# Performance work log

Measured on AMD Instinct MI355X. Metric: run time of the kernel, lower is better.

## Reference

```python
import jax, jax.numpy as jnp
import numpy as np

N = 100000
E = 640000
D = 128      # node_dim == edge_dim
H = 256      # conv MLP hidden dim
EPS = 1e-5


def _ln(x, g, b):
    mu = jnp.mean(x, axis=-1, keepdims=True)
    var = jnp.var(x, axis=-1, keepdims=True)
    return (x - mu) * jax.lax.rsqrt(var + EPS) * g + b


def _conv_mlp(x, W1, b1, g1, be1, W2, b2, g2, be2):
    h = _ln(x @ W1 + b1, g1, be1)          # (N, H)
    h = jax.nn.relu(h)
    return _ln(h @ W2 + b2, g2, be2)        # (N, D)


def setup_inputs() -> dict:
    key = jax.random.key(0)
    ks = jax.random.split(key, 6)
    s1 = 1.0 / np.sqrt(D)
    s2 = 1.0 / np.sqrt(H)
    return {
        "x": jax.random.normal(ks[0], (N, D), dtype=jnp.float32),
        "edge_index": jax.random.randint(ks[1], (2, E), 0, N, dtype=jnp.int32),
        "edge_attr": jax.random.normal(ks[2], (E, D), dtype=jnp.float32),
        "W1": jax.random.uniform(ks[3], (D, H), jnp.float32, -s1, s1),
        "b1": jnp.zeros((H,), jnp.float32),
        "g1": jnp.ones((H,), jnp.float32),
        "be1": jnp.zeros((H,), jnp.float32),
        "W2": jax.random.uniform(ks[4], (H, D), jnp.float32, -s2, s2),
        "b2": jnp.zeros((D,), jnp.float32),
        "g2": jnp.ones((D,), jnp.float32),
        "be2": jnp.zeros((D,), jnp.float32),
        "g_out": jnp.ones((D,), jnp.float32),
        "b_out": jnp.zeros((D,), jnp.float32),
    }


def reference(x, edge_index, edge_attr, W1, b1, g1, be1, W2, b2, g2, be2, g_out, b_out):
    # Conv(h[w]) for all nodes once, then gather per edge (vectorized form of
    # the per-node/per-neighbor loops in the torch module).
    conv = _conv_mlp(x, W1, b1, g1, be1, W2, b2, g2, be2)   # (N, D)
    src, dst = edge_index[0], edge_index[1]
    msgs = conv[dst] * edge_attr                            # (E, D): Conv(h[w]) * e[v,w]
    agg = jax.ops.segment_sum(msgs, src, num_segments=N)    # scatter-add into v
    return _ln(agg + x, g_out, b_out)
```

## Files before the change

kernel.cpp:

```cpp
#include <hip/hip_runtime.h>

constexpr int D = 128;
constexpr int H = 256;
constexpr float EPS = 1e-5f;

typedef __attribute__((ext_vector_type(8))) __bf16  bf16x8;
typedef __attribute__((ext_vector_type(4))) float   f32x4;

static __device__ __forceinline__ unsigned short f2bfu(float f) {
    unsigned u = __float_as_uint(f);
    return (unsigned short)((u + 0x7FFFu + ((u >> 16) & 1u)) >> 16);
}
static __device__ __forceinline__ float bf2f(unsigned short u) {
    return __uint_as_float((unsigned)u << 16);
}

static __device__ __forceinline__ f32x4 mfma16x16x32(bf16x8 a, bf16x8 b, f32x4 c) {
    return __builtin_amdgcn_mfma_f32_16x16x32_bf16(a, b, c, 0, 0, 0);
}

__global__ __launch_bounds__(256) void pack_w_kernel(
    const float* __restrict__ W, unsigned short* __restrict__ Wp, int K, int Ncols)
{
    int e = blockIdx.x * 256 + threadIdx.x;
    if (e >= K * Ncols) return;
    int i  = e & 7;
    int l  = (e >> 3) & 63;
    int jt = e >> 9;
    int nt = K >> 5;
    int j  = jt / nt;
    int t  = jt - j * nt;
    int k  = 32 * t + ((l >> 4) << 3) + i;
    int c  = 16 * j + (l & 15);
    Wp[e] = f2bfu(W[(size_t)k * Ncols + c]);
}

__global__ __launch_bounds__(256) void conv_mlp_mfma(
    const float* __restrict__ x,
    const unsigned short* __restrict__ W1p, const float* __restrict__ b1,
    const float* __restrict__ g1, const float* __restrict__ be1,
    const unsigned short* __restrict__ W2p, const float* __restrict__ b2,
    const float* __restrict__ g2, const float* __restrict__ be2,
    unsigned short* __restrict__ convb, int N)
{
    __shared__ unsigned short Hs[64 * 256];
    const int wv   = threadIdx.x >> 6;
    const int lane = threadIdx.x & 63;
    const int rrow = lane & 15;
    const int kgrp = lane >> 4;
    const int r0   = blockIdx.x * 64 + wv * 16;

    int arow = r0 + rrow; if (arow >= N) arow = N - 1;
    const float* xr = x + (size_t)arow * D + kgrp * 8;
    bf16x8 A1[4];
    #pragma unroll
    for (int t = 0; t < 4; ++t) {
        float4 fa = *(const float4*)(xr + t * 32);
        float4 fb = *(const float4*)(xr + t * 32 + 4);
        bf16x8 a;
        a[0] = (__bf16)fa.x; a[1] = (__bf16)fa.y; a[2] = (__bf16)fa.z; a[3] = (__bf16)fa.w;
        a[4] = (__bf16)fb.x; a[5] = (__bf16)fb.y; a[6] = (__bf16)fb.z; a[7] = (__bf16)fb.w;
        A1[t] = a;
    }

    f32x4 acc[16];
    #pragma unroll
    for (int j = 0; j < 16; ++j) acc[j] = (f32x4){0.f, 0.f, 0.f, 0.f};
    const bf16x8* w1f = (const bf16x8*)W1p;
    #pragma unroll
    for (int j = 0; j < 16; ++j) {
        #pragma unroll
        for (int t = 0; t < 4; ++t) {
            bf16x8 B = w1f[(j * 4 + t) * 64 + lane];
            acc[j] = mfma16x16x32(A1[t], B, acc[j]);
        }
    }

    float b1r[16], g1r[16], be1r[16];
    #pragma unroll
    for (int j = 0; j < 16; ++j) {
        int c = 16 * j + rrow;
        b1r[j] = b1[c]; g1r[j] = g1[c]; be1r[j] = be1[c];
    }

    float s1[4] = {0,0,0,0}, s2[4] = {0,0,0,0};
    #pragma unroll
    for (int j = 0; j < 16; ++j) {
        #pragma unroll
        for (int r = 0; r < 4; ++r) {
            float v = acc[j][r] + b1r[j];
            acc[j][r] = v;
            s1[r] += v; s2[r] += v * v;
        }
    }
    #pragma unroll
    for (int m = 1; m < 16; m <<= 1) {
        #pragma unroll
        for (int r = 0; r < 4; ++r) {
            s1[r] += __shfl_xor(s1[r], m);
            s2[r] += __shfl_xor(s2[r], m);
        }
    }

    #pragma unroll
    for (int r = 0; r < 4; ++r) {
        float mu  = s1[r] * (1.f / H);
        float var = s2[r] * (1.f / H) - mu * mu;
        float rs  = rsqrtf(var + EPS);
        int row = wv * 16 + kgrp * 4 + r;
        #pragma unroll
        for (int j = 0; j < 16; ++j) {
            float h = fmaxf((acc[j][r] - mu) * rs * g1r[j] + be1r[j], 0.f);
            int byte = (row << 9) + ((16 * j + rrow) << 1);
            byte ^= (row & 15) << 4;
            *(unsigned short*)((char*)Hs + byte) = f2bfu(h);
        }
    }

    bf16x8 A2[8];
    #pragma unroll
    for (int t = 0; t < 8; ++t) {
        int row  = wv * 16 + rrow;
        int byte = (row << 9) + ((t * 32 + kgrp * 8) << 1);
        byte ^= (row & 15) << 4;
        A2[t] = *(const bf16x8*)((const char*)Hs + byte);
    }

    f32x4 acc2[8];
    #pragma unroll
    for (int j = 0; j < 8; ++j) acc2[j] = (f32x4){0.f, 0.f, 0.f, 0.f};
    const bf16x8* w2f = (const bf16x8*)W2p;
    #pragma unroll
    for (int j = 0; j < 8; ++j) {
        #pragma unroll
        for (int t = 0; t < 8; ++t) {
            bf16x8 B = w2f[(j * 8 + t) * 64 + lane];
            acc2[j] = mfma16x16x32(A2[t], B, acc2[j]);
        }
    }

    float b2r[8], g2r[8], be2r[8];
    #pragma unroll
    for (int j = 0; j < 8; ++j) {
        int c = 16 * j + rrow;
        b2r[j] = b2[c]; g2r[j] = g2[c]; be2r[j] = be2[c];
    }

    float u1[4] = {0,0,0,0}, u2[4] = {0,0,0,0};
    #pragma unroll
    for (int j = 0; j < 8; ++j) {
        #pragma unroll
        for (int r = 0; r < 4; ++r) {
            float v = acc2[j][r] + b2r[j];
            acc2[j][r] = v;
            u1[r] += v; u2[r] += v * v;
        }
    }
    #pragma unroll
    for (int m = 1; m < 16; m <<= 1) {
        #pragma unroll
        for (int r = 0; r < 4; ++r) {
            u1[r] += __shfl_xor(u1[r], m);
            u2[r] += __shfl_xor(u2[r], m);
        }
    }
    #pragma unroll
    for (int r = 0; r < 4; ++r) {
        float mu  = u1[r] * (1.f / D);
        float var = u2[r] * (1.f / D) - mu * mu;
        float rs  = rsqrtf(var + EPS);
        int grow = r0 + kgrp * 4 + r;
        if (grow < N) {
            #pragma unroll
            for (int j = 0; j < 8; ++j) {
                float o = (acc2[j][r] - mu) * rs * g2r[j] + be2r[j];
                convb[(size_t)grow * D + 16 * j + rrow] = f2bfu(o);
            }
        }
    }
}

__global__ __launch_bounds__(256) void zero_int_kernel(int* __restrict__ p, int n) {
    int i = blockIdx.x * blockDim.x + threadIdx.x;
    if (i < n) p[i] = 0;
}

__global__ __launch_bounds__(256) void hist_kernel(
    const int* __restrict__ eidx, int* __restrict__ counts, int E)
{
    int e = blockIdx.x * blockDim.x + threadIdx.x;
    if (e < E) atomicAdd(&counts[eidx[e]], 1);
}

__global__ __launch_bounds__(256) void scan1_kernel(
    const int* __restrict__ counts, int* __restrict__ row_start,
    int* __restrict__ bsums, int N)
{
    __shared__ int sd[256];
    int t  = threadIdx.x;
    int i0 = blockIdx.x * 1024 + t * 4;
    int c0 = (i0+0 < N) ? counts[i0+0] : 0;
    int c1 = (i0+1 < N) ? counts[i0+1] : 0;
    int c2 = (i0+2 < N) ? counts[i0+2] : 0;
    int c3 = (i0+3 < N) ? counts[i0+3] : 0;
    int s  = c0 + c1 + c2 + c3;
    sd[t] = s;
    __syncthreads();
    #pragma unroll
    for (int off = 1; off < 256; off <<= 1) {
        int v = (t >= off) ? sd[t - off] : 0;
        __syncthreads();
        sd[t] += v;
        __syncthreads();
    }
    int ex = sd[t] - s;
    if (i0+0 < N) row_start[i0+0] = ex;
    if (i0+1 < N) row_start[i0+1] = ex + c0;
    if (i0+2 < N) row_start[i0+2] = ex + c0 + c1;
    if (i0+3 < N) row_start[i0+3] = ex + c0 + c1 + c2;
    if (t == 255) bsums[blockIdx.x] = sd[255];
}

__global__ __launch_bounds__(128) void scan2_kernel(int* __restrict__ bsums, int NB)
{
    __shared__ int sd[128];
    int t = threadIdx.x;
    int v = (t < NB) ? bsums[t] : 0;
    sd[t] = v;
    __syncthreads();
    #pragma unroll
    for (int off = 1; off < 128; off <<= 1) {
        int u = (t >= off) ? sd[t - off] : 0;
        __syncthreads();
        sd[t] += u;
        __syncthreads();
    }
    if (t < NB) bsums[t] = sd[t] - v;
}

__global__ __launch_bounds__(256) void scan3_kernel(
    int* __restrict__ row_start, const int* __restrict__ bsums,
    int* __restrict__ cursor, int N)
{
    int i = blockIdx.x * blockDim.x + threadIdx.x;
    if (i < N) {
        int r = row_start[i] + bsums[i >> 10];
        row_start[i] = r;
        cursor[i]    = r;
    }
}

__global__ __launch_bounds__(256) void fill_kernel(
    const int* __restrict__ eidx, int* __restrict__ cursor,
    int2* __restrict__ edat, int E)
{
    int e = blockIdx.x * blockDim.x + threadIdx.x;
    if (e < E) {
        int s = eidx[e];
        int p = atomicAdd(&cursor[s], 1);
        edat[p] = make_int2(e, eidx[E + e]);
    }
}

__global__ __launch_bounds__(256) void gather_ln_kernel(
    const float* __restrict__ x, const unsigned short* __restrict__ convb,
    const float* __restrict__ eattr,
    const int* __restrict__ row_start, const int2* __restrict__ edat,
    const float* __restrict__ g, const float* __restrict__ b,
    float* __restrict__ out, int N, int E)
{
    int node = blockIdx.x * 4 + (threadIdx.x >> 6);
    if (node >= N) return;
    int lane = threadIdx.x & 63;
    int half = lane >> 5;
    int c4   = (lane & 31) * 4;

    float4 acc = make_float4(0.f, 0.f, 0.f, 0.f);
    int je = (node + 1 < N) ? row_start[node + 1] : E;
    int j  = row_start[node] + half;

    for (; j + 2 < je; j += 4) {
        int2 ea = edat[j];
        int2 eb = edat[j + 2];
        ushort4 ca = *(const ushort4*)(convb + (size_t)ea.y * D + c4);
        float4  aa = *(const float4*) (eattr + (size_t)ea.x * D + c4);
        ushort4 cb = *(const ushort4*)(convb + (size_t)eb.y * D + c4);
        float4  ab = *(const float4*) (eattr + (size_t)eb.x * D + c4);
        acc.x += bf2f(ca.x) * aa.x; acc.y += bf2f(ca.y) * aa.y;
        acc.z += bf2f(ca.z) * aa.z; acc.w += bf2f(ca.w) * aa.w;
        acc.x += bf2f(cb.x) * ab.x; acc.y += bf2f(cb.y) * ab.y;
        acc.z += bf2f(cb.z) * ab.z; acc.w += bf2f(cb.w) * ab.w;
    }
    if (j < je) {
        int2 ea = edat[j];
        ushort4 ca = *(const ushort4*)(convb + (size_t)ea.y * D + c4);
        float4  aa = *(const float4*) (eattr + (size_t)ea.x * D + c4);
        acc.x += bf2f(ca.x) * aa.x; acc.y += bf2f(ca.y) * aa.y;
        acc.z += bf2f(ca.z) * aa.z; acc.w += bf2f(ca.w) * aa.w;
    }

    if (half == 0) {
        float4 xv = *(const float4*)(x + (size_t)node * D + c4);
        acc.x += xv.x; acc.y += xv.y; acc.z += xv.z; acc.w += xv.w;
    }
    acc.x += __shfl_xor(acc.x, 32);
    acc.y += __shfl_xor(acc.y, 32);
    acc.z += __shfl_xor(acc.z, 32);
    acc.w += __shfl_xor(acc.w, 32);

    float s1 = acc.x + acc.y + acc.z + acc.w;
    float s2 = acc.x*acc.x + acc.y*acc.y + acc.z*acc.z + acc.w*acc.w;
    #pragma unroll
    for (int o = 1; o < 32; o <<= 1) {
        s1 += __shfl_xor(s1, o);
        s2 += __shfl_xor(s2, o);
    }
    float mu  = s1 * (1.f / D);
    float var = s2 * (1.f / D) - mu * mu;
    float rs  = rsqrtf(var + EPS);
    if (half == 0) {
        float4 gv = *(const float4*)(g + c4);
        float4 bv = *(const float4*)(b + c4);
        float4 o4;
        o4.x = (acc.x - mu) * rs * gv.x + bv.x;
        o4.y = (acc.y - mu) * rs * gv.y + bv.y;
        o4.z = (acc.z - mu) * rs * gv.z + bv.z;
        o4.w = (acc.w - mu) * rs * gv.w + bv.w;
        *(float4*)(out + (size_t)node * D + c4) = o4;
    }
}

extern "C" void kernel_launch(void* const* d_in, const int* in_sizes, int n_in,
                              void* d_out, int out_size, void* d_ws, size_t ws_size,
                              hipStream_t stream) {
    const float* x     = (const float*)d_in[0];
    const int*   eidx  = (const int*)  d_in[1];
    const float* eattr = (const float*)d_in[2];
    const float* W1    = (const float*)d_in[3];
    const float* b1    = (const float*)d_in[4];
    const float* g1    = (const float*)d_in[5];
    const float* be1   = (const float*)d_in[6];
    const float* W2    = (const float*)d_in[7];
    const float* b2    = (const float*)d_in[8];
    const float* g2    = (const float*)d_in[9];
    const float* be2   = (const float*)d_in[10];
    const float* g_out = (const float*)d_in[11];
    const float* b_out = (const float*)d_in[12];

    const int N = in_sizes[0] / D;
    const int E = in_sizes[1] / 2;

    float* out = (float*)d_out;

    auto align_up = [](size_t v) { return (v + 255) & ~(size_t)255; };
    size_t convB = align_up((size_t)N * D * sizeof(unsigned short));
    size_t cntB  = align_up((size_t)N * sizeof(int));
    size_t rsB   = align_up((size_t)N * sizeof(int));
    size_t bsB   = align_up(128 * sizeof(int));
    size_t edB   = align_up((size_t)E * sizeof(int2));
    size_t w1B   = align_up((size_t)D * H * sizeof(unsigned short));

    char* w = (char*)d_ws;
    unsigned short* convb     = (unsigned short*)(w);
    int*            counts    = (int*)(w + convB);
    int*            row_start = (int*)(w + convB + cntB);
    int*            bsums     = (int*)(w + convB + cntB + rsB);
    int2*           edat      = (int2*)(w + convB + cntB + rsB + bsB);
    unsigned short* W1p       = (unsigned short*)(w + convB + cntB + rsB + bsB + edB);
    unsigned short* W2p       = (unsigned short*)(w + convB + cntB + rsB + bsB + edB + w1B);

    pack_w_kernel<<<(D * H + 255) / 256, 256, 0, stream>>>(W1, W1p, D, H);
    pack_w_kernel<<<(H * D + 255) / 256, 256, 0, stream>>>(W2, W2p, H, D);

    conv_mlp_mfma<<<(N + 63) / 64, 256, 0, stream>>>(
        x, W1p, b1, g1, be1, W2p, b2, g2, be2, convb, N);

    zero_int_kernel<<<(N + 255) / 256, 256, 0, stream>>>(counts, N);
    hist_kernel<<<(E + 255) / 256, 256, 0, stream>>>(eidx, counts, E);
    int NB = (N + 1023) / 1024;
    scan1_kernel<<<NB, 256, 0, stream>>>(counts, row_start, bsums, N);
    scan2_kernel<<<1, 128, 0, stream>>>(bsums, NB);
    scan3_kernel<<<(N + 255) / 256, 256, 0, stream>>>(row_start, bsums, counts, N);
    fill_kernel<<<(E + 255) / 256, 256, 0, stream>>>(eidx, counts, edat, E);

    gather_ln_kernel<<<(N + 3) / 4, 256, 0, stream>>>(
        x, convb, eattr, row_start, edat, g_out, b_out, out, N, E);
}
```

Before: 230.2 us.

## Fuse weight packing, zeroing, conv+histogram and scan into fewer launches

Weight packing and zeroing of the count buffer are merged into one prep kernel. The conv MLP and the edge-degree histogram now run as one horizontally fused kernel, with blocks dispatched by block index, so the histogram overlaps the MLP. The three-pass prefix scan is replaced by a single 1024-thread block in which each thread serially scans a contiguous chunk, and the cursor now aliases the counts buffer. This cuts the number of launches, but the single-block scan serializes about 100 strided loads per thread, and the histogram blocks now carry the conv kernel's LDS allocation.

New measurement: 432.2 us. 87.8% more time.

```diff
diff --git a/kernel.cpp b/kernel.cpp
--- a/kernel.cpp
+++ b/kernel.cpp
@@ -19,11 +19,9 @@
     return __builtin_amdgcn_mfma_f32_16x16x32_bf16(a, b, c, 0, 0, 0);
 }
 
-__global__ __launch_bounds__(256) void pack_w_kernel(
-    const float* __restrict__ W, unsigned short* __restrict__ Wp, int K, int Ncols)
-{
-    int e = blockIdx.x * 256 + threadIdx.x;
-    if (e >= K * Ncols) return;
+static __device__ __forceinline__ void pack_w_elem(
+    const float* __restrict__ W, unsigned short* __restrict__ Wp, int K, int Ncols, int e)
+{
     int i  = e & 7;
     int l  = (e >> 3) & 63;
     int jt = e >> 9;
@@ -35,20 +33,36 @@
     Wp[e] = f2bfu(W[(size_t)k * Ncols + c]);
 }
 
-__global__ __launch_bounds__(256) void conv_mlp_mfma(
+__global__ __launch_bounds__(256) void prep_kernel(
+    const float* __restrict__ W1, unsigned short* __restrict__ W1p,
+    const float* __restrict__ W2, unsigned short* __restrict__ W2p,
+    int* __restrict__ counts, int N)
+{
+    int b = blockIdx.x;
+    if (b < 128) {
+        pack_w_elem(W1, W1p, D, H, b * 256 + threadIdx.x);
+    } else if (b < 256) {
+        pack_w_elem(W2, W2p, H, D, (b - 128) * 256 + threadIdx.x);
+    } else {
+        int i = (b - 256) * 256 + threadIdx.x;
+        if (i < N) counts[i] = 0;
+    }
+}
+
+static __device__ void conv_body(
+    unsigned short* __restrict__ Hs,
     const float* __restrict__ x,
     const unsigned short* __restrict__ W1p, const float* __restrict__ b1,
     const float* __restrict__ g1, const float* __restrict__ be1,
     const unsigned short* __restrict__ W2p, const float* __restrict__ b2,
     const float* __restrict__ g2, const float* __restrict__ be2,
-    unsigned short* __restrict__ convb, int N)
-{
-    __shared__ unsigned short Hs[64 * 256];
+    unsigned short* __restrict__ convb, int N, int cblk)
+{
     const int wv   = threadIdx.x >> 6;
     const int lane = threadIdx.x & 63;
     const int rrow = lane & 15;
     const int kgrp = lane >> 4;
-    const int r0   = blockIdx.x * 64 + wv * 16;
+    const int r0   = cblk * 64 + wv * 16;
 
     int arow = r0 + rrow; if (arow >= N) arow = N - 1;
     const float* xr = x + (size_t)arow * D + kgrp * 8;
@@ -169,7 +183,7 @@
         float mu  = u1[r] * (1.f / D);
         float var = u2[r] * (1.f / D) - mu * mu;
         float rs  = rsqrtf(var + EPS);
-        int grow = r0 + kgrp * 4 + r;
+        int grow = cblk * 64 + kgrp * 4 + r + (threadIdx.x >> 6) * 16;
         if (grow < N) {
             #pragma unroll
             for (int j = 0; j < 8; ++j) {
@@ -180,73 +194,50 @@
     }
 }
 
-__global__ __launch_bounds__(256) void zero_int_kernel(int* __restrict__ p, int n) {
-    int i = blockIdx.x * blockDim.x + threadIdx.x;
-    if (i < n) p[i] = 0;
-}
-
-__global__ __launch_bounds__(256) void hist_kernel(
-    const int* __restrict__ eidx, int* __restrict__ counts, int E)
-{
-    int e = blockIdx.x * blockDim.x + threadIdx.x;
-    if (e < E) atomicAdd(&counts[eidx[e]], 1);
-}
-
-__global__ __launch_bounds__(256) void scan1_kernel(
+__global__ __launch_bounds__(256) void conv_hist_kernel(
+    const float* __restrict__ x,
+    const unsigned short* __restrict__ W1p, const float* __restrict__ b1,
+    const float* __restrict__ g1, const float* __restrict__ be1,
+    const unsigned short* __restrict__ W2p, const float* __restrict__ b2,
+    const float* __restrict__ g2, const float* __restrict__ be2,
+    unsigned short* __restrict__ convb, int N,
+    const int* __restrict__ eidx, int* __restrict__ counts, int E, int convBlocks)
+{
+    __shared__ unsigned short Hs[64 * 256];
+    if ((int)blockIdx.x < convBlocks) {
+        conv_body(Hs, x, W1p, b1, g1, be1, W2p, b2, g2, be2, convb, N, blockIdx.x);
+    } else {
+        int e = (blockIdx.x - convBlocks) * 256 + threadIdx.x;
+        if (e < E) atomicAdd(&counts[eidx[e]], 1);
+    }
+}
+
+__global__ __launch_bounds__(1024) void scan_kernel(
     const int* __restrict__ counts, int* __restrict__ row_start,
-    int* __restrict__ bsums, int N)
-{
-    __shared__ int sd[256];
+    int* __restrict__ cursor, int N)
+{
+    __shared__ int sd[1024];
     int t  = threadIdx.x;
-    int i0 = blockIdx.x * 1024 + t * 4;
-    int c0 = (i0+0 < N) ? counts[i0+0] : 0;
-    int c1 = (i0+1 < N) ? counts[i0+1] : 0;
-    int c2 = (i0+2 < N) ? counts[i0+2] : 0;
-    int c3 = (i0+3 < N) ? counts[i0+3] : 0;
-    int s  = c0 + c1 + c2 + c3;
+    int CH = (N + 1023) >> 10;
+    int i0 = t * CH;
+    int i1 = i0 + CH; if (i1 > N) i1 = N;
+    int s = 0;
+    for (int i = i0; i < i1; ++i) s += counts[i];
     sd[t] = s;
     __syncthreads();
     #pragma unroll
-    for (int off = 1; off < 256; off <<= 1) {
+    for (int off = 1; off < 1024; off <<= 1) {
         int v = (t >= off) ? sd[t - off] : 0;
         __syncthreads();
         sd[t] += v;
         __syncthreads();
     }
-    int ex = sd[t] - s;
-    if (i0+0 < N) row_start[i0+0] = ex;
-    if (i0+1 < N) row_start[i0+1] = ex + c0;
-    if (i0+2 < N) row_start[i0+2] = ex + c0 + c1;
-    if (i0+3 < N) row_start[i0+3] = ex + c0 + c1 + c2;
-    if (t == 255) bsums[blockIdx.x] = sd[255];
-}
-
-__global__ __launch_bounds__(128) void scan2_kernel(int* __restrict__ bsums, int NB)
-{
-    __shared__ int sd[128];
-    int t = threadIdx.x;
-    int v = (t < NB) ? bsums[t] : 0;
-    sd[t] = v;
-    __syncthreads();
-    #pragma unroll
-    for (int off = 1; off < 128; off <<= 1) {
-        int u = (t >= off) ? sd[t - off] : 0;
-        __syncthreads();
-        sd[t] += u;
-        __syncthreads();
-    }
-    if (t < NB) bsums[t] = sd[t] - v;
-}
-
-__global__ __launch_bounds__(256) void scan3_kernel(
-    int* __restrict__ row_start, const int* __restrict__ bsums,
-    int* __restrict__ cursor, int N)
-{
-    int i = blockIdx.x * blockDim.x + threadIdx.x;
-    if (i < N) {
-        int r = row_start[i] + bsums[i >> 10];
-        row_start[i] = r;
-        cursor[i]    = r;
+    int run = sd[t] - s;
+    for (int i = i0; i < i1; ++i) {
+        int c = counts[i];
+        row_start[i] = run;
+        cursor[i]    = run;
+        run += c;
     }
 }
 
@@ -364,23 +355,20 @@
     unsigned short* convb     = (unsigned short*)(w);
     int*            counts    = (int*)(w + convB);
     int*            row_start = (int*)(w + convB + cntB);
-    int*            bsums     = (int*)(w + convB + cntB + rsB);
     int2*           edat      = (int2*)(w + convB + cntB + rsB + bsB);
     unsigned short* W1p       = (unsigned short*)(w + convB + cntB + rsB + bsB + edB);
     unsigned short* W2p       = (unsigned short*)(w + convB + cntB + rsB + bsB + edB + w1B);
 
-    pack_w_kernel<<<(D * H + 255) / 256, 256, 0, stream>>>(W1, W1p, D, H);
-    pack_w_kernel<<<(H * D + 255) / 256, 256, 0, stream>>>(W2, W2p, H, D);
-
-    conv_mlp_mfma<<<(N + 63) / 64, 256, 0, stream>>>(
-        x, W1p, b1, g1, be1, W2p, b2, g2, be2, convb, N);
-
-    zero_int_kernel<<<(N + 255) / 256, 256, 0, stream>>>(counts, N);
-    hist_kernel<<<(E + 255) / 256, 256, 0, stream>>>(eidx, counts, E);
-    int NB = (N + 1023) / 1024;
-    scan1_kernel<<<NB, 256, 0, stream>>>(counts, row_start, bsums, N);
-    scan2_kernel<<<1, 128, 0, stream>>>(bsums, NB);
-    scan3_kernel<<<(N + 255) / 256, 256, 0, stream>>>(row_start, bsums, counts, N);
+    int zeroBlocks = (N + 255) / 256;
+    prep_kernel<<<256 + zeroBlocks, 256, 0, stream>>>(W1, W1p, W2, W2p, counts, N);
+
+    int convBlocks = (N + 63) / 64;
+    int histBlocks = (E + 255) / 256;
+    conv_hist_kernel<<<convBlocks + histBlocks, 256, 0, stream>>>(
+        x, W1p, b1, g1, be1, W2p, b2, g2, be2, convb, N, eidx, counts, E, convBlocks);
+
+    scan_kernel<<<1, 1024, 0, stream>>>(counts, row_start, counts, N);
+
     fill_kernel<<<(E + 255) / 256, 256, 0, stream>>>(eidx, counts, edat, E);
 
     gather_ln_kernel<<<(N + 3) / 4, 256, 0, stream>>>(
```
